# Kernel tuning notes

Hardware: AMD Instinct MI355X
Metric: run time of the kernel (lower is better)

## Reference

```python
import jax, jax.numpy as jnp
import numpy as np
import math

H, Dh, S = 8, 64, 3          # heads, dim per head, samples factor
B, T, N, K = 2, 12, 512, 16  # batch, time, nodes, local-adj width
F = H * Dh                   # features = 512
SN = int(S * math.log2(N))   # Sampled_Nodes = 27
EPS = 1e-5


def setup_inputs() -> dict:
    key = jax.random.key(0)
    ks = jax.random.split(key, 22)
    sc = 1.0 / math.sqrt(F)
    W = lambda k: jax.random.normal(k, (F, F), jnp.float32) * sc
    bb = lambda k: jax.random.normal(k, (F,), jnp.float32) * 0.01
    return {
        "x": jax.random.normal(ks[0], (B, T, N, F), jnp.float32),
        "spa_eigvalue": jax.random.normal(ks[1], (F,), jnp.float32) * 0.1,
        "spa_eigvec": jax.random.normal(ks[2], (N, F), jnp.float32) * 0.1,
        "tem_eigvalue": jax.random.normal(ks[3], (F,), jnp.float32) * 0.1,
        "tem_eigvec": jax.random.normal(ks[4], (N, F), jnp.float32) * 0.1,
        "localadj": jax.random.randint(ks[5], (N, K), 0, N),
        "Wq": W(ks[6]), "bq": bb(ks[7]),
        "Wk": W(ks[8]), "bk": bb(ks[9]),
        "Wv": W(ks[10]), "bv": bb(ks[11]),
        "Wo": W(ks[12]), "bo": bb(ks[13]),
        "w_proj": jax.random.normal(ks[14], (K,), jnp.float32) / math.sqrt(K),
        "b_proj": jax.random.normal(ks[15], (), jnp.float32) * 0.01,
        "gamma": jnp.ones((F,), jnp.float32),
        "beta": jnp.zeros((F,), jnp.float32),
        "W1": W(ks[16]), "b1": bb(ks[17]),
        "W2": W(ks[18]), "b2": bb(ks[19]),
    }


def _lin(v, Wm, bv):  # torch nn.Linear: y = x @ W^T + b, W is [out, in]
    return jnp.einsum('...i,oi->...o', v, Wm) + bv


def _ln(v, g=None, b=None):  # LayerNorm over last dim, eps=1e-5
    mu = jnp.mean(v, -1, keepdims=True)
    var = jnp.var(v, -1, keepdims=True)
    y = (v - mu) * jax.lax.rsqrt(var + EPS)
    return y * g + b if g is not None else y


def reference(x, spa_eigvalue, spa_eigvec, tem_eigvalue, tem_eigvec, localadj,
              Wq, bq, Wk, bk, Wv, bv, Wo, bo, w_proj, b_proj,
              gamma, beta, W1, b1, W2, b2):
    # eigvec @ diag(eigval) == row-wise scaling
    x_ = x + (spa_eigvec * spa_eigvalue + tem_eigvec * tem_eigvalue)
    to_heads = lambda v: v.reshape(B, T, N, H, Dh).transpose(3, 0, 1, 2, 4)  # [H,B,T,N,Dh]
    Qh = to_heads(_lin(x_, Wq, bq))
    Kh = to_heads(_lin(x_, Wk, bk))
    Vh = to_heads(_lin(x_, Wv, bv))
    # local-adjacency K sampling: [H,B,T,N,K,Dh]
    Ks = Kh[:, :, :, localadj, :]
    qks = jnp.einsum('hbtnd,hbtnkd->hbtnk', Qh, Ks)
    # importance score per query node via learned projection over K neighbors
    M = jnp.einsum('hbtnk,k->hbtn', qks, w_proj) + b_proj
    _, m_top = jax.lax.top_k(M, SN)                              # [H,B,T,SN]
    Qr = jnp.take_along_axis(Qh, m_top[..., None], axis=3)       # [H,B,T,SN,Dh]
    scores = jnp.einsum('hbtsd,hbtnd->hbtsn', Qr, Kh) / math.sqrt(Dh)
    attn = jax.nn.softmax(scores, axis=-1)                       # [H,B,T,SN,N]
    cp = jnp.argmax(attn, axis=-2)                               # best sampled query per key node [H,B,T,N]
    val = jnp.einsum('hbtsn,hbtnd->hbtsd', attn, Vh)             # [H,B,T,SN,Dh]
    out = jnp.take_along_axis(val, cp[..., None], axis=3)        # [H,B,T,N,Dh]
    out = out.transpose(1, 2, 3, 0, 4).reshape(B, T, N, F)       # merge heads
    v = _ln(_lin(out, Wo, bo), gamma, beta)
    h = jax.nn.relu(_lin(v, W1, b1))
    h = _lin(h, W2, b2) + v
    return _ln(h)
```

## Files before the change

kernel.cpp:

```cpp
#include <hip/hip_runtime.h>
#include <math.h>

#define H_    8
#define DH    64
#define NN    512
#define KADJ  16
#define FF    512
#define BTOT  24
#define ROWS  12288
#define SN_   27
#define EPS_  1e-5f

typedef short short8 __attribute__((ext_vector_type(8)));
typedef float f32x4  __attribute__((ext_vector_type(4)));

__device__ __forceinline__ ushort f2bf(float x) {
    uint u = __float_as_uint(x);
    u += 0x7FFFu + ((u >> 16) & 1u);
    return (ushort)(u >> 16);
}
__device__ __forceinline__ float bf2f(ushort h) {
    return __uint_as_float(((uint)h) << 16);
}

__device__ __forceinline__ void gload_lds16(const ushort* g, ushort* l) {
    __builtin_amdgcn_global_load_lds(
        (const __attribute__((address_space(1))) unsigned int*)g,
        (__attribute__((address_space(3))) unsigned int*)l,
        16, 0, 0);
}

__global__ __launch_bounds__(256) void add_pos_bf16(
    const float* __restrict__ x,
    const float* __restrict__ spa_val, const float* __restrict__ spa_vec,
    const float* __restrict__ tem_val, const float* __restrict__ tem_vec,
    ushort* __restrict__ xh, ushort* __restrict__ xl)
{
    int i = blockIdx.x * 256 + threadIdx.x;
    int f4  = i & 127;
    int row = i >> 7;
    int n   = row & (NN - 1);

    float4 xv = reinterpret_cast<const float4*>(x)[i];
    float4 sv = reinterpret_cast<const float4*>(spa_vec)[n * 128 + f4];
    float4 tv = reinterpret_cast<const float4*>(tem_vec)[n * 128 + f4];
    float4 se = reinterpret_cast<const float4*>(spa_val)[f4];
    float4 te = reinterpret_cast<const float4*>(tem_val)[f4];
    float r0 = xv.x + sv.x * se.x + tv.x * te.x;
    float r1 = xv.y + sv.y * se.y + tv.y * te.y;
    float r2 = xv.z + sv.z * se.z + tv.z * te.z;
    float r3 = xv.w + sv.w * se.w + tv.w * te.w;
    ushort h0 = f2bf(r0), h1 = f2bf(r1), h2 = f2bf(r2), h3 = f2bf(r3);
    reinterpret_cast<ushort4*>(xh)[i] = make_ushort4(h0, h1, h2, h3);
    reinterpret_cast<ushort4*>(xl)[i] = make_ushort4(
        f2bf(r0 - bf2f(h0)), f2bf(r1 - bf2f(h1)),
        f2bf(r2 - bf2f(h2)), f2bf(r3 - bf2f(h3)));
}

__global__ __launch_bounds__(256) void wconv_kernel(
    const float* __restrict__ w0, const float* __restrict__ w1,
    const float* __restrict__ w2, const float* __restrict__ w3,
    const float* __restrict__ w4, const float* __restrict__ w5,
    ushort* __restrict__ whi, ushort* __restrict__ wlo)
{
    const int wi = blockIdx.y;
    const float* W = wi == 0 ? w0 : wi == 1 ? w1 : wi == 2 ? w2 :
                     wi == 3 ? w3 : wi == 4 ? w4 : w5;
    int i = blockIdx.x * 256 + threadIdx.x;
    float4 v = reinterpret_cast<const float4*>(W)[i];
    ushort h0 = f2bf(v.x), h1 = f2bf(v.y), h2 = f2bf(v.z), h3 = f2bf(v.w);
    reinterpret_cast<ushort4*>(whi + (size_t)wi * 262144)[i] =
        make_ushort4(h0, h1, h2, h3);
    if (wi < 2) {
        reinterpret_cast<ushort4*>(wlo + (size_t)wi * 262144)[i] =
            make_ushort4(f2bf(v.x - bf2f(h0)), f2bf(v.y - bf2f(h1)),
                         f2bf(v.z - bf2f(h2)), f2bf(v.w - bf2f(h3)));
    }
}

#define GBM 64
#define GBN 128

template <int SPLIT, int EPI, int OUT>
__global__ __launch_bounds__(256, 2) void gemm_mfma2(
    const ushort* __restrict__ Ah, const ushort* __restrict__ Al,
    const ushort* __restrict__ Wh, const ushort* __restrict__ Wl,
    const float* __restrict__ bias, const float* __restrict__ addsrc,
    float* __restrict__ Cf, ushort* __restrict__ Cb, ushort* __restrict__ Cl)
{
    __shared__ ushort sA[GBM * 64];
    __shared__ ushort sB[GBN * 64];

    const int nx  = gridDim.x >> 3;
    const int bid = blockIdx.x;
    const int lt  = (bid & 7) * nx + (bid >> 3);
    const int rowBase = (lt >> 2) * GBM;
    const int colBase = (lt & 3) * GBN;

    const int tid  = threadIdx.x;
    const int lane = tid & 63;
    const int wid  = tid >> 6;
    const int q    = lane >> 4;
    const int fr   = lane & 15;
    const int wm   = wid & 1;
    const int wn   = wid >> 1;

    const int kadv = SPLIT ? 32 : 64;
    const ushort* asrc[2];
    const ushort* bsrc[4];
    #pragma unroll
    for (int c = 0; c < 2; ++c) {
        const int p   = wid * 2048 + c * 1024 + lane * 16;
        const int row = p >> 7;
        const int ss  = ((p >> 4) & 7) ^ (row & 7);
        if (!SPLIT)
            asrc[c] = Ah + (size_t)(rowBase + row) * FF + ss * 8;
        else
            asrc[c] = (ss < 4)
                ? Ah + (size_t)(rowBase + row) * FF + ss * 8
                : Al + (size_t)(rowBase + row) * FF + (ss - 4) * 8;
    }
    #pragma unroll
    for (int c = 0; c < 4; ++c) {
        const int p   = wid * 4096 + c * 1024 + lane * 16;
        const int row = p >> 7;
        const int ss  = ((p >> 4) & 7) ^ (row & 7);
        if (!SPLIT)
            bsrc[c] = Wh + (size_t)(colBase + row) * FF + ss * 8;
        else
            bsrc[c] = (ss < 4)
                ? Wh + (size_t)(colBase + row) * FF + ss * 8
                : Wl + (size_t)(colBase + row) * FF + (ss - 4) * 8;
    }

    f32x4 acc[2][4];
    #pragma unroll
    for (int mi = 0; mi < 2; ++mi)
        #pragma unroll
        for (int ni = 0; ni < 4; ++ni) acc[mi][ni] = (f32x4){0.f, 0.f, 0.f, 0.f};

    const int NSTEP = SPLIT ? 16 : 8;
    const int swz = fr & 7;

    for (int step = 0; step < NSTEP; ++step) {
        #pragma unroll
        for (int c = 0; c < 2; ++c) {
            gload_lds16(asrc[c], &sA[wid * 1024 + c * 512]);
            asrc[c] += kadv;
        }
        #pragma unroll
        for (int c = 0; c < 4; ++c) {
            gload_lds16(bsrc[c], &sB[wid * 2048 + c * 512]);
            bsrc[c] += kadv;
        }
        __syncthreads();

        if (!SPLIT) {
            #pragma unroll
            for (int ksub = 0; ksub < 2; ++ksub) {
                const int kq = ksub * 4 + q;
                short8 af[2], bf[4];
                #pragma unroll
                for (int mi = 0; mi < 2; ++mi)
                    af[mi] = *(const short8*)&sA[(wm * 32 + mi * 16 + fr) * 64 +
                                                 ((kq ^ swz) << 3)];
                #pragma unroll
                for (int ni = 0; ni < 4; ++ni)
                    bf[ni] = *(const short8*)&sB[(wn * 64 + ni * 16 + fr) * 64 +
                                                 ((kq ^ swz) << 3)];
                #pragma unroll
                for (int mi = 0; mi < 2; ++mi)
                    #pragma unroll
                    for (int ni = 0; ni < 4; ++ni)
                        acc[mi][ni] = __builtin_amdgcn_mfma_f32_16x16x32_bf16(
                            af[mi], bf[ni], acc[mi][ni], 0, 0, 0);
            }
        } else {
            short8 ah[2], bh[4], t[4];
            #pragma unroll
            for (int mi = 0; mi < 2; ++mi)
                ah[mi] = *(const short8*)&sA[(wm * 32 + mi * 16 + fr) * 64 +
                                             ((q ^ swz) << 3)];
            #pragma unroll
            for (int ni = 0; ni < 4; ++ni)
                bh[ni] = *(const short8*)&sB[(wn * 64 + ni * 16 + fr) * 64 +
                                             ((q ^ swz) << 3)];
            #pragma unroll
            for (int mi = 0; mi < 2; ++mi)
                #pragma unroll
                for (int ni = 0; ni < 4; ++ni)
                    acc[mi][ni] = __builtin_amdgcn_mfma_f32_16x16x32_bf16(
                        ah[mi], bh[ni], acc[mi][ni], 0, 0, 0);
            #pragma unroll
            for (int ni = 0; ni < 4; ++ni)
                t[ni] = *(const short8*)&sB[(wn * 64 + ni * 16 + fr) * 64 +
                                            (((q + 4) ^ swz) << 3)];
            #pragma unroll
            for (int mi = 0; mi < 2; ++mi)
                #pragma unroll
                for (int ni = 0; ni < 4; ++ni)
                    acc[mi][ni] = __builtin_amdgcn_mfma_f32_16x16x32_bf16(
                        ah[mi], t[ni], acc[mi][ni], 0, 0, 0);
            #pragma unroll
            for (int mi = 0; mi < 2; ++mi)
                t[mi] = *(const short8*)&sA[(wm * 32 + mi * 16 + fr) * 64 +
                                            (((q + 4) ^ swz) << 3)];
            #pragma unroll
            for (int mi = 0; mi < 2; ++mi)
                #pragma unroll
                for (int ni = 0; ni < 4; ++ni)
                    acc[mi][ni] = __builtin_amdgcn_mfma_f32_16x16x32_bf16(
                        t[mi], bh[ni], acc[mi][ni], 0, 0, 0);
        }
        __syncthreads();
    }

    #pragma unroll
    for (int mi = 0; mi < 2; ++mi)
        #pragma unroll
        for (int ni = 0; ni < 4; ++ni) {
            const int col = colBase + wn * 64 + ni * 16 + fr;
            const float bcol = bias[col];
            #pragma unroll
            for (int r = 0; r < 4; ++r) {
                const int row = rowBase + wm * 32 + mi * 16 + q * 4 + r;
                float v = acc[mi][ni][r] + bcol;
                if (EPI == 1) v = fmaxf(v, 0.0f);
                if (EPI == 2) v += addsrc[(size_t)row * FF + col];
                const size_t idx = (size_t)row * FF + col;
                if (OUT == 0) Cf[idx] = v;
                if (OUT == 1) Cb[idx] = f2bf(v);
                if (OUT == 2) {
                    ushort hh = f2bf(v);
                    Cb[idx] = hh;
                    Cl[idx] = f2bf(v - bf2f(hh));
                }
            }
        }
}

__global__ __launch_bounds__(256) void qks_M_kernel(
    const ushort* __restrict__ Qh, const ushort* __restrict__ Ql,
    const ushort* __restrict__ Kh, const ushort* __restrict__ Kl,
    const int* __restrict__ adj, const float* __restrict__ w_proj,
    const float* __restrict__ b_proj, float* __restrict__ Mout)
{
    const int w = blockIdx.x * 4 + (threadIdx.x >> 6);
    const int lane = threadIdx.x & 63;
    const int n   = w & (NN - 1);
    const int hbt = w >> 9;
    const int h   = hbt / BTOT;
    const int bt  = hbt % BTOT;

    float s = 0.0f;
    #pragma unroll
    for (int k = 0; k < KADJ; ++k) {
        const int j = adj[n * KADJ + k];
        const size_t idx = ((size_t)(bt * NN + j)) * FF + h * DH + lane;
        s += w_proj[k] * (bf2f(Kh[idx]) + bf2f(Kl[idx]));
    }
    const size_t qidx = ((size_t)(bt * NN + n)) * FF + h * DH + lane;
    float t = (bf2f(Qh[qidx]) + bf2f(Ql[qidx])) * s;
    #pragma unroll
    for (int o = 32; o; o >>= 1) t += __shfl_xor(t, o);
    if (lane == 0) Mout[(size_t)hbt * NN + n] = t + b_proj[0];
}

__global__ __launch_bounds__(64) void topk_kernel(
    const float* __restrict__ M, int* __restrict__ mtop)
{
    const int g = blockIdx.x;
    __shared__ float vals[NN];
    const int lane = threadIdx.x;
    for (int i = lane; i < NN; i += 64) vals[i] = M[(size_t)g * NN + i];
    __syncthreads();

    for (int s = 0; s < SN_; ++s) {
        float bv = -INFINITY;
        int bi = 1 << 30;
        for (int i = lane; i < NN; i += 64) {
            float v = vals[i];
            if (v > bv || (v == bv && i < bi)) { bv = v; bi = i; }
        }
        #pragma unroll
        for (int o = 32; o; o >>= 1) {
            float ov = __shfl_xor(bv, o);
            int   oi = __shfl_xor(bi, o);
            if (ov > bv || (ov == bv && oi < bi)) { bv = ov; bi = oi; }
        }
        if (lane == 0) {
            mtop[g * SN_ + s] = bi;
            vals[bi] = -INFINITY;
        }
        __syncthreads();
    }
}

__global__ __launch_bounds__(1024) void fused_attn(
    const ushort* __restrict__ Qh, const ushort* __restrict__ Ql,
    const ushort* __restrict__ Kh, const ushort* __restrict__ Kl,
    const ushort* __restrict__ Vb, const int* __restrict__ mtop,
    ushort* __restrict__ attnout)
{
    __shared__ ushort P_lds[32 * 512];
    __shared__ ushort Vt_lds[64 * 512];
    __shared__ float red0[16][32];
    __shared__ float red1[16][32];
    __shared__ float val2[2][32][68];
    __shared__ int   cp_lds[NN];
    __shared__ int   mt[32];

    const int g = blockIdx.x;
    const int h = g / BTOT, bt = g % BTOT;
    const int tid = threadIdx.x;
    const int wave = tid >> 6, lane = tid & 63;
    const int q = lane >> 4, c = lane & 15;
    const size_t base_bt = (size_t)bt * NN * FF;
    const int hcol = h * DH;

    if (tid < 32) mt[tid] = mtop[g * SN_ + (tid < SN_ ? tid : 0)];
    __syncthreads();

    const int n0 = wave * 32;
    short8 bfh[2][2], bfl[2][2];
    #pragma unroll
    for (int nt = 0; nt < 2; ++nt) {
        const size_t kp = base_bt + (size_t)(n0 + nt * 16 + c) * FF + hcol + q * 8;
        #pragma unroll
        for (int ks = 0; ks < 2; ++ks) {
            bfh[nt][ks] = *(const short8*)&Kh[kp + ks * 32];
            bfl[nt][ks] = *(const short8*)&Kl[kp + ks * 32];
        }
    }

    ushort4 vreg[2][4];
    #pragma unroll
    for (int i = 0; i < 2; ++i) {
        const int u  = tid + i * 1024;
        const int d4 = u & 15, ng = u >> 4;
        #pragma unroll
        for (int ii = 0; ii < 4; ++ii)
            vreg[i][ii] = *(const ushort4*)&Vb[base_bt +
                (size_t)(ng * 4 + ii) * FF + hcol + d4 * 4];
    }

    short8 afh[2][2], afl[2][2];
    #pragma unroll
    for (int m = 0; m < 2; ++m) {
        const int grow = mt[m * 16 + c];
        const size_t qp = base_bt + (size_t)grow * FF + hcol + q * 8;
        #pragma unroll
        for (int ks = 0; ks < 2; ++ks) {
            afh[m][ks] = *(const short8*)&Qh[qp + ks * 32];
            afl[m][ks] = *(const short8*)&Ql[qp + ks * 32];
        }
    }

    f32x4 sc[2][2];
    #pragma unroll
    for (int m = 0; m < 2; ++m)
        #pragma unroll
        for (int nt = 0; nt < 2; ++nt) sc[m][nt] = (f32x4){0.f, 0.f, 0.f, 0.f};
    #pragma unroll
    for (int ks = 0; ks < 2; ++ks)
        #pragma unroll
        for (int m = 0; m < 2; ++m)
            #pragma unroll
            for (int nt = 0; nt < 2; ++nt) {
                sc[m][nt] = __builtin_amdgcn_mfma_f32_16x16x32_bf16(
                    afh[m][ks], bfh[nt][ks], sc[m][nt], 0, 0, 0);
                sc[m][nt] = __builtin_amdgcn_mfma_f32_16x16x32_bf16(
                    afh[m][ks], bfl[nt][ks], sc[m][nt], 0, 0, 0);
                sc[m][nt] = __builtin_amdgcn_mfma_f32_16x16x32_bf16(
                    afl[m][ks], bfh[nt][ks], sc[m][nt], 0, 0, 0);
            }
    #pragma unroll
    for (int m = 0; m < 2; ++m)
        #pragma unroll
        for (int nt = 0; nt < 2; ++nt)
            #pragma unroll
            for (int r = 0; r < 4; ++r) sc[m][nt][r] *= 0.125f;

    float rmax[2][4];
    #pragma unroll
    for (int m = 0; m < 2; ++m)
        #pragma unroll
        for (int r = 0; r < 4; ++r)
            rmax[m][r] = fmaxf(sc[m][0][r], sc[m][1][r]);
    #pragma unroll
    for (int off = 1; off <= 8; off <<= 1)
        #pragma unroll
        for (int m = 0; m < 2; ++m)
            #pragma unroll
            for (int r = 0; r < 4; ++r)
                rmax[m][r] = fmaxf(rmax[m][r], __shfl_xor(rmax[m][r], off));
    if (c == 0) {
        #pragma unroll
        for (int m = 0; m < 2; ++m)
            #pragma unroll
            for (int r = 0; r < 4; ++r)
                red0[wave][m * 16 + q * 4 + r] = rmax[m][r];
    }
    __syncthreads();
    float gmax[2][4];
    #pragma unroll
    for (int m = 0; m < 2; ++m)
        #pragma unroll
        for (int r = 0; r < 4; ++r) {
            const int row = m * 16 + q * 4 + r;
            float v = red0[0][row];
            #pragma unroll
            for (int w = 1; w < 16; ++w) v = fmaxf(v, red0[w][row]);
            gmax[m][r] = v;
        }

    float rsum[2][4] = {};
    #pragma unroll
    for (int m = 0; m < 2; ++m)
        #pragma unroll
        for (int nt = 0; nt < 2; ++nt)
            #pragma unroll
            for (int r = 0; r < 4; ++r) {
                float e = expf(sc[m][nt][r] - gmax[m][r]);
                sc[m][nt][r] = e;
                rsum[m][r] += e;
            }
    #pragma unroll
    for (int off = 1; off <= 8; off <<= 1)
        #pragma unroll
        for (int m = 0; m < 2; ++m)
            #pragma unroll
            for (int r = 0; r < 4; ++r)
                rsum[m][r] += __shfl_xor(rsum[m][r], off);
    if (c == 0) {
        #pragma unroll
        for (int m = 0; m < 2; ++m)
            #pragma unroll
            for (int r = 0; r < 4; ++r)
                red1[wave][m * 16 + q * 4 + r] = rsum[m][r];
    }
    __syncthreads();
    #pragma unroll
    for (int m = 0; m < 2; ++m)
        #pragma unroll
        for (int r = 0; r < 4; ++r) {
            const int row = m * 16 + q * 4 + r;
            float s = red1[0][row];
            #pragma unroll
            for (int w = 1; w < 16; ++w) s += red1[w][row];
            const float inv = 1.0f / s;
            #pragma unroll
            for (int nt = 0; nt < 2; ++nt) sc[m][nt][r] *= inv;
        }

    #pragma unroll
    for (int nt = 0; nt < 2; ++nt) {
        float bv = -INFINITY;
        int bi = 1 << 30;
        #pragma unroll
        for (int m = 0; m < 2; ++m)
            #pragma unroll
            for (int r = 0; r < 4; ++r) {
                const int row = m * 16 + q * 4 + r;
                if (row < SN_) {
                    float v = sc[m][nt][r];
                    if (v > bv) { bv = v; bi = row; }
                }
            }
        #pragma unroll
        for (int off = 16; off <= 32; off <<= 1) {
            float ov = __shfl_xor(bv, off);
            int   oi = __shfl_xor(bi, off);
            if (ov > bv || (ov == bv && oi < bi)) { bv = ov; bi = oi; }
        }
        if (q == 0) cp_lds[n0 + nt * 16 + c] = bi;
    }

    #pragma unroll
    for (int m = 0; m < 2; ++m)
        #pragma unroll
        for (int nt = 0; nt < 2; ++nt)
            #pragma unroll
            for (int r = 0; r < 4; ++r) {
                const int row = m * 16 + q * 4 + r;
                const int col = n0 + nt * 16 + c;
                P_lds[(row * 512 + col) ^ ((row & 7) << 3)] = f2bf(sc[m][nt][r]);
            }

    #pragma unroll
    for (int i = 0; i < 2; ++i) {
        const int u  = tid + i * 1024;
        const int d4 = u & 15, ng = u >> 4;
        const int n0v = ng * 4;
        #pragma unroll
        for (int j = 0; j < 4; ++j) {
            const int d = d4 * 4 + j;
            ushort4 t;
            t.x = ((const ushort*)&vreg[i][0])[j];
            t.y = ((const ushort*)&vreg[i][1])[j];
            t.z = ((const ushort*)&vreg[i][2])[j];
            t.w = ((const ushort*)&vreg[i][3])[j];
            *(ushort4*)&Vt_lds[(d * 512 + n0v) ^ ((d & 7) << 3)] = t;
        }
    }
    __syncthreads();

    const int kh = wave >> 3, rem = wave & 7;
    const int msel = rem >> 2, dt = rem & 3;
    const int dcol = dt * 16 + c;
    const int prow = msel * 16 + c;
    const int pswz = (prow & 7) << 3;
    const int vswz = (dcol & 7) << 3;
    f32x4 acc = (f32x4){0.f, 0.f, 0.f, 0.f};
    #pragma unroll
    for (int ks8 = 0; ks8 < 8; ++ks8) {
        const int kstep = kh * 8 + ks8;
        short8 a = *(const short8*)&P_lds[(prow * 512 + kstep * 32 + q * 8) ^ pswz];
        short8 b = *(const short8*)&Vt_lds[(dcol * 512 + kstep * 32 + q * 8) ^ vswz];
        acc = __builtin_amdgcn_mfma_f32_16x16x32_bf16(a, b, acc, 0, 0, 0);
    }
    #pragma unroll
    for (int r = 0; r < 4; ++r)
        val2[kh][msel * 16 + q * 4 + r][dt * 16 + c] = acc[r];
    __syncthreads();

    #pragma unroll
    for (int pass = 0; pass < 4; ++pass) {
        const int n  = pass * 128 + (tid >> 3);
        const int s  = cp_lds[n];
        const int d0 = (tid & 7) * 8;
        float vr[8];
        #pragma unroll
        for (int j = 0; j < 8; ++j)
            vr[j] = val2[0][s][d0 + j] + val2[1][s][d0 + j];
        uint4 u;
        u.x = (uint)f2bf(vr[0]) | ((uint)f2bf(vr[1]) << 16);
        u.y = (uint)f2bf(vr[2]) | ((uint)f2bf(vr[3]) << 16);
        u.z = (uint)f2bf(vr[4]) | ((uint)f2bf(vr[5]) << 16);
        u.w = (uint)f2bf(vr[6]) | ((uint)f2bf(vr[7]) << 16);
        *(uint4*)(attnout + base_bt + (size_t)n * FF + hcol + d0) = u;
    }
}

template <int AFFINE, int BFOUT>
__global__ __launch_bounds__(256) void ln_kernel(
    const float* __restrict__ X, const float* __restrict__ g,
    const float* __restrict__ b, float* __restrict__ Yf,
    ushort* __restrict__ Yb, int rows)
{
    const int row = blockIdx.x * 4 + (threadIdx.x >> 6);
    if (row >= rows) return;
    const int lane = threadIdx.x & 63;
    const float4* x4 = reinterpret_cast<const float4*>(X + (size_t)row * FF);
    float4 a = x4[lane];
    float4 c = x4[lane + 64];
    float s = a.x + a.y + a.z + a.w + c.x + c.y + c.z + c.w;
    float q = a.x * a.x + a.y * a.y + a.z * a.z + a.w * a.w +
              c.x * c.x + c.y * c.y + c.z * c.z + c.w * c.w;
    #pragma unroll
    for (int o = 32; o; o >>= 1) {
        s += __shfl_xor(s, o);
        q += __shfl_xor(q, o);
    }
    const float mu   = s * (1.0f / FF);
    const float var  = q * (1.0f / FF) - mu * mu;
    const float rstd = 1.0f / sqrtf(var + EPS_);

    float4 ya, yc;
    ya.x = (a.x - mu) * rstd; ya.y = (a.y - mu) * rstd;
    ya.z = (a.z - mu) * rstd; ya.w = (a.w - mu) * rstd;
    yc.x = (c.x - mu) * rstd; yc.y = (c.y - mu) * rstd;
    yc.z = (c.z - mu) * rstd; yc.w = (c.w - mu) * rstd;
    if (AFFINE) {
        float4 ga = reinterpret_cast<const float4*>(g)[lane];
        float4 gc = reinterpret_cast<const float4*>(g)[lane + 64];
        float4 ba = reinterpret_cast<const float4*>(b)[lane];
        float4 bc = reinterpret_cast<const float4*>(b)[lane + 64];
        ya.x = ya.x * ga.x + ba.x; ya.y = ya.y * ga.y + ba.y;
        ya.z = ya.z * ga.z + ba.z; ya.w = ya.w * ga.w + ba.w;
        yc.x = yc.x * gc.x + bc.x; yc.y = yc.y * gc.y + bc.y;
        yc.z = yc.z * gc.z + bc.z; yc.w = yc.w * gc.w + bc.w;
    }
    float4* y4 = reinterpret_cast<float4*>(Yf + (size_t)row * FF);
    y4[lane]      = ya;
    y4[lane + 64] = yc;
    if (BFOUT) {
        ushort4* yb = reinterpret_cast<ushort4*>(Yb + (size_t)row * FF);
        yb[lane] = make_ushort4(f2bf(ya.x), f2bf(ya.y), f2bf(ya.z), f2bf(ya.w));
        yb[lane + 64] = make_ushort4(f2bf(yc.x), f2bf(yc.y), f2bf(yc.z), f2bf(yc.w));
    }
}

extern "C" void kernel_launch(void* const* d_in, const int* in_sizes, int n_in,
                              void* d_out, int out_size, void* d_ws, size_t ws_size,
                              hipStream_t stream)
{
    const float* x       = (const float*)d_in[0];
    const float* spa_val = (const float*)d_in[1];
    const float* spa_vec = (const float*)d_in[2];
    const float* tem_val = (const float*)d_in[3];
    const float* tem_vec = (const float*)d_in[4];
    const int*   adj     = (const int*)  d_in[5];
    const float* Wq = (const float*)d_in[6];  const float* bq = (const float*)d_in[7];
    const float* Wk = (const float*)d_in[8];  const float* bk = (const float*)d_in[9];
    const float* Wv = (const float*)d_in[10]; const float* bv = (const float*)d_in[11];
    const float* Wo = (const float*)d_in[12]; const float* bo = (const float*)d_in[13];
    const float* w_proj = (const float*)d_in[14];
    const float* b_proj = (const float*)d_in[15];
    const float* gamma  = (const float*)d_in[16];
    const float* beta   = (const float*)d_in[17];
    const float* W1 = (const float*)d_in[18]; const float* b1 = (const float*)d_in[19];
    const float* W2 = (const float*)d_in[20]; const float* b2 = (const float*)d_in[21];

    float* out = (float*)d_out;

    const size_t R = (size_t)ROWS * FF;

    ushort* ws_u = (ushort*)d_ws;
    ushort* bufQh = ws_u;
    ushort* bufQl = ws_u + R;
    ushort* bufKh = ws_u + 2 * R;
    ushort* bufKl = ws_u + 3 * R;
    ushort* bufVb = ws_u + 4 * R;
    ushort* whi   = ws_u + 5 * R;
    ushort* wlo   = whi + 6 * 262144;
    float*  Mbuf  = (float*)(wlo + 2 * 262144);
    int*    mtop  = (int*)(Mbuf + (size_t)H_ * BTOT * NN);

    float* o_f32 = (float*)bufQh;
    float* v_f32 = (float*)bufKh;
    float* h2_f32 = (float*)bufQh;

    ushort* xh  = (ushort*)d_out;
    ushort* xl  = xh + R;
    ushort* attnout = xh;
    ushort* vbf = xl;
    ushort* h1b = xh;

    add_pos_bf16<<<(ROWS * FF / 4) / 256, 256, 0, stream>>>(
        x, spa_val, spa_vec, tem_val, tem_vec, xh, xl);

    wconv_kernel<<<dim3(256, 6), 256, 0, stream>>>(Wq, Wk, Wv, Wo, W1, W2, whi, wlo);

    const int NG = (ROWS / GBM) * (FF / GBN);
    gemm_mfma2<1, 0, 2><<<NG, 256, 0, stream>>>(xh, xl, whi, wlo, bq, nullptr,
                                                nullptr, bufQh, bufQl);
    gemm_mfma2<1, 0, 2><<<NG, 256, 0, stream>>>(xh, xl, whi + 262144, wlo + 262144,
                                                bk, nullptr, nullptr, bufKh, bufKl);
    gemm_mfma2<0, 0, 1><<<NG, 256, 0, stream>>>(xh, nullptr, whi + 2 * 262144, nullptr,
                                                bv, nullptr, nullptr, bufVb, nullptr);

    qks_M_kernel<<<(H_ * BTOT * NN) / 4, 256, 0, stream>>>(
        bufQh, bufQl, bufKh, bufKl, adj, w_proj, b_proj, Mbuf);
    topk_kernel<<<H_ * BTOT, 64, 0, stream>>>(Mbuf, mtop);

    fused_attn<<<H_ * BTOT, 1024, 0, stream>>>(
        bufQh, bufQl, bufKh, bufKl, bufVb, mtop, attnout);

    gemm_mfma2<0, 0, 0><<<NG, 256, 0, stream>>>(attnout, nullptr, whi + 3 * 262144,
                                                nullptr, bo, nullptr, o_f32, nullptr, nullptr);
    ln_kernel<1, 1><<<ROWS / 4, 256, 0, stream>>>(o_f32, gamma, beta, v_f32, vbf, ROWS);
    gemm_mfma2<0, 1, 1><<<NG, 256, 0, stream>>>(vbf, nullptr, whi + 4 * 262144, nullptr,
                                                b1, nullptr, nullptr, h1b, nullptr);
    gemm_mfma2<0, 2, 0><<<NG, 256, 0, stream>>>(h1b, nullptr, whi + 5 * 262144, nullptr,
                                                b2, v_f32, h2_f32, nullptr, nullptr);
    ln_kernel<0, 0><<<ROWS / 4, 256, 0, stream>>>(h2_f32, nullptr, nullptr, out, nullptr, ROWS);
}
```

Baseline: 248.1 us.

## Fuse neighbor score computation with top-k selection using LDS-staged K tile

Merges the qks/M scoring kernel and the top-k kernel into one kernel with one block per head/batch/time group. Each block stages that group's K head slice (hi+lo combined as fp32) in LDS, so neighbor gathers read LDS instead of scattered global memory. M is kept in LDS instead of a global buffer, which also removes one launch. The cost is only 192 blocks of 1024 threads with 128KB+ of LDS each, lower parallelism than the old 24576-wave scoring kernel, and a serial top-k done by a single wave.

```diff
diff --git a/kernel.cpp b/kernel.cpp
--- a/kernel.cpp
+++ b/kernel.cpp
@@ -239,60 +239,98 @@
         }
 }
 
-__global__ __launch_bounds__(256) void qks_M_kernel(
+__global__ __launch_bounds__(1024) void qks_topk_kernel(
     const ushort* __restrict__ Qh, const ushort* __restrict__ Ql,
     const ushort* __restrict__ Kh, const ushort* __restrict__ Kl,
     const int* __restrict__ adj, const float* __restrict__ w_proj,
-    const float* __restrict__ b_proj, float* __restrict__ Mout)
+    const float* __restrict__ b_proj, int* __restrict__ mtop)
 {
-    const int w = blockIdx.x * 4 + (threadIdx.x >> 6);
-    const int lane = threadIdx.x & 63;
-    const int n   = w & (NN - 1);
-    const int hbt = w >> 9;
-    const int h   = hbt / BTOT;
-    const int bt  = hbt % BTOT;
-
-    float s = 0.0f;
-    #pragma unroll
-    for (int k = 0; k < KADJ; ++k) {
-        const int j = adj[n * KADJ + k];
-        const size_t idx = ((size_t)(bt * NN + j)) * FF + h * DH + lane;
-        s += w_proj[k] * (bf2f(Kh[idx]) + bf2f(Kl[idx]));
-    }
-    const size_t qidx = ((size_t)(bt * NN + n)) * FF + h * DH + lane;
-    float t = (bf2f(Qh[qidx]) + bf2f(Ql[qidx])) * s;
-    #pragma unroll
-    for (int o = 32; o; o >>= 1) t += __shfl_xor(t, o);
-    if (lane == 0) Mout[(size_t)hbt * NN + n] = t + b_proj[0];
-}
-
-__global__ __launch_bounds__(64) void topk_kernel(
-    const float* __restrict__ M, int* __restrict__ mtop)
-{
+    __shared__ float sK[NN * DH];
+    __shared__ float M_lds[NN];
+
     const int g = blockIdx.x;
-    __shared__ float vals[NN];
-    const int lane = threadIdx.x;
-    for (int i = lane; i < NN; i += 64) vals[i] = M[(size_t)g * NN + i];
+    const int h = g / BTOT, bt = g % BTOT;
+    const int tid = threadIdx.x;
+    const size_t headbase = (size_t)(bt * NN) * FF + h * DH;
+
+    #pragma unroll
+    for (int it = 0; it < 8; ++it) {
+        const int u  = tid + it * 1024;
+        const int j  = u >> 4;
+        const int dq = (u & 15) * 4;
+        const size_t gidx = headbase + (size_t)j * FF + dq;
+        ushort4 hv = *(const ushort4*)&Kh[gidx];
+        ushort4 lv = *(const ushort4*)&Kl[gidx];
+        float4 f;
+        f.x = bf2f(hv.x) + bf2f(lv.x);
+        f.y = bf2f(hv.y) + bf2f(lv.y);
+        f.z = bf2f(hv.z) + bf2f(lv.z);
+        f.w = bf2f(hv.w) + bf2f(lv.w);
+        *(float4*)&sK[j * DH + dq] = f;
+    }
+
+    float wv[KADJ];
+    #pragma unroll
+    for (int k = 0; k < KADJ; ++k) wv[k] = w_proj[k];
+    const float b0 = b_proj[0];
+
     __syncthreads();
 
-    for (int s = 0; s < SN_; ++s) {
-        float bv = -INFINITY;
-        int bi = 1 << 30;
-        for (int i = lane; i < NN; i += 64) {
-            float v = vals[i];
-            if (v > bv || (v == bv && i < bi)) { bv = v; bi = i; }
-        }
-        #pragma unroll
-        for (int o = 32; o; o >>= 1) {
-            float ov = __shfl_xor(bv, o);
-            int   oi = __shfl_xor(bi, o);
-            if (ov > bv || (ov == bv && oi < bi)) { bv = ov; bi = oi; }
-        }
-        if (lane == 0) {
-            mtop[g * SN_ + s] = bi;
-            vals[bi] = -INFINITY;
-        }
-        __syncthreads();
+    const int wave = tid >> 6, lane = tid & 63;
+    const int nsub = lane >> 4;
+    const int d4   = (lane & 15) * 4;
+    for (int i = 0; i < 8; ++i) {
+        const int n = wave * 32 + i * 4 + nsub;
+        int4 aj[4];
+        #pragma unroll
+        for (int p = 0; p < 4; ++p)
+            aj[p] = *(const int4*)&adj[n * KADJ + p * 4];
+        f32x4 s4 = (f32x4){0.f, 0.f, 0.f, 0.f};
+        #pragma unroll
+        for (int p = 0; p < 4; ++p) {
+            const int* jp = (const int*)&aj[p];
+            #pragma unroll
+            for (int e = 0; e < 4; ++e) {
+                f32x4 kv = *(const f32x4*)&sK[jp[e] * DH + d4];
+                const float w = wv[p * 4 + e];
+                s4[0] += w * kv[0]; s4[1] += w * kv[1];
+                s4[2] += w * kv[2]; s4[3] += w * kv[3];
+            }
+        }
+        const size_t qidx = headbase + (size_t)n * FF + d4;
+        ushort4 qh = *(const ushort4*)&Qh[qidx];
+        ushort4 ql = *(const ushort4*)&Ql[qidx];
+        float t = (bf2f(qh.x) + bf2f(ql.x)) * s4[0]
+                + (bf2f(qh.y) + bf2f(ql.y)) * s4[1]
+                + (bf2f(qh.z) + bf2f(ql.z)) * s4[2]
+                + (bf2f(qh.w) + bf2f(ql.w)) * s4[3];
+        #pragma unroll
+        for (int o = 1; o <= 8; o <<= 1) t += __shfl_xor(t, o);
+        if ((lane & 15) == 0) M_lds[n] = t + b0;
+    }
+    __syncthreads();
+
+    if (wave == 0) {
+        for (int s = 0; s < SN_; ++s) {
+            float bv = -INFINITY;
+            int bi = 1 << 30;
+            #pragma unroll
+            for (int ii = 0; ii < 8; ++ii) {
+                const int i = lane + ii * 64;
+                float v = M_lds[i];
+                if (v > bv || (v == bv && i < bi)) { bv = v; bi = i; }
+            }
+            #pragma unroll
+            for (int o = 32; o; o >>= 1) {
+                float ov = __shfl_xor(bv, o);
+                int   oi = __shfl_xor(bi, o);
+                if (ov > bv || (ov == bv && oi < bi)) { bv = ov; bi = oi; }
+            }
+            bi = __shfl(bi, 0);
+            if (lane == 0) mtop[g * SN_ + s] = bi;
+            if (lane == 0) M_lds[bi] = -INFINITY;
+            __builtin_amdgcn_s_waitcnt(0);
+        }
     }
 }
 
@@ -624,8 +662,7 @@
     ushort* bufVb = ws_u + 4 * R;
     ushort* whi   = ws_u + 5 * R;
     ushort* wlo   = whi + 6 * 262144;
-    float*  Mbuf  = (float*)(wlo + 2 * 262144);
-    int*    mtop  = (int*)(Mbuf + (size_t)H_ * BTOT * NN);
+    int*    mtop  = (int*)(wlo + 2 * 262144);
 
     float* o_f32 = (float*)bufQh;
     float* v_f32 = (float*)bufKh;
@@ -650,9 +687,8 @@
     gemm_mfma2<0, 0, 1><<<NG, 256, 0, stream>>>(xh, nullptr, whi + 2 * 262144, nullptr,
                                                 bv, nullptr, nullptr, bufVb, nullptr);
 
-    qks_M_kernel<<<(H_ * BTOT * NN) / 4, 256, 0, stream>>>(
-        bufQh, bufQl, bufKh, bufKl, adj, w_proj, b_proj, Mbuf);
-    topk_kernel<<<H_ * BTOT, 64, 0, stream>>>(Mbuf, mtop);
+    qks_topk_kernel<<<H_ * BTOT, 1024, 0, stream>>>(
+        bufQh, bufQl, bufKh, bufKl, adj, w_proj, b_proj, mtop);
 
     fused_attn<<<H_ * BTOT, 1024, 0, stream>>>(
         bufQh, bufQl, bufKh, bufKl, bufVb, mtop, attnout);
```

New measurement: 211.7 us. -14.7%, faster.
